# Kernel optimization log

Measured on AMD Instinct MI355X. Metric: run time of the kernel, lower is better.

The kernel has to match this reference:

```python
import jax, jax.numpy as jnp
import numpy as np

B, S, D, H = 4, 2048, 1024, 16
DK = D // H


def setup_inputs() -> dict:
    key = jax.random.key(0)
    ks = jax.random.split(key, 7)
    scale = 1.0 / np.sqrt(D)
    return {
        "query": jax.random.normal(ks[0], (B, S, D), dtype=jnp.float32),
        "key": jax.random.normal(ks[1], (B, S, D), dtype=jnp.float32),
        "value": jax.random.normal(ks[2], (B, S, D), dtype=jnp.float32),
        "mask": jnp.ones((B, S), dtype=bool),
        "w_q": jax.random.normal(ks[3], (D, D), dtype=jnp.float32) * scale,
        "w_k": jax.random.normal(ks[4], (D, D), dtype=jnp.float32) * scale,
        "w_v": jax.random.normal(ks[5], (D, D), dtype=jnp.float32) * scale,
        "w_o": jax.random.normal(ks[6], (D, D), dtype=jnp.float32) * scale,
    }


def reference(query, key, value, mask, w_q, w_k, w_v, w_o):
    b, tgt, d = query.shape
    src = key.shape[1]
    # torch Linear (no bias): x @ W.T
    Q = (query @ w_q.T).reshape(b, tgt, H, DK).transpose(0, 2, 1, 3)  # (B,H,T,dk)
    K = (key @ w_k.T).reshape(b, src, H, DK).transpose(0, 2, 1, 3)
    V = (value @ w_v.T).reshape(b, src, H, DK).transpose(0, 2, 1, 3)
    scores = jnp.einsum('bhtd,bhsd->bhts', Q, K) / np.sqrt(DK)  # (B,H,T,S)
    m = mask[:, None, None, :]  # (B,1,1,S)
    scores = jnp.where(m, scores, -jnp.inf)
    attn = jax.nn.softmax(scores, axis=-1)
    out = jnp.einsum('bhts,bhsd->bhtd', attn, V)
    out = out.transpose(0, 2, 1, 3).reshape(b, tgt, d)
    return out @ w_o.T
```

## Files before the change

### kernel.cpp

```cpp
#include <hip/hip_runtime.h>
#include <hip/hip_bf16.h>

#define NB 4
#define NS 2048
#define ND 1024
#define NH 16
#define NDK 64
#define GM 8192
#define GK 1024
#define GN 1024

typedef __bf16 bf16;
typedef __bf16 bf16x4 __attribute__((ext_vector_type(4)));
typedef __bf16 bf16x8 __attribute__((ext_vector_type(8)));
typedef float  f32x4  __attribute__((ext_vector_type(4)));
typedef float  f32x16 __attribute__((ext_vector_type(16)));
typedef unsigned u32x4 __attribute__((ext_vector_type(4)));

__device__ __forceinline__ void gl16(const void* g, void* l) {
  __builtin_amdgcn_global_load_lds((__attribute__((address_space(1))) void*)g,
                                   (__attribute__((address_space(3))) void*)l,
                                   16, 0, 0);
}

__device__ __forceinline__ unsigned cvtpk(float a, float b) {
  unsigned r;
  asm("v_cvt_pk_bf16_f32 %0, %1, %2" : "=v"(r) : "v"(a), "v"(b));
  return r;
}
__device__ __forceinline__ void plswap(unsigned &x, unsigned &y) {
  asm("v_permlane32_swap_b32 %0, %1" : "+v"(x), "+v"(y));
}
__device__ __forceinline__ float max3(float a, float b, float c) {
  float r;
  asm("v_max3_f32 %0, %1, %2, %3" : "=v"(r) : "v"(a), "v"(b), "v"(c));
  return r;
}
__device__ __forceinline__ float rexp2(float x) {
  float r;
  asm("v_exp_f32 %0, %1" : "=v"(r) : "v"(x));
  return r;
}

__device__ __forceinline__ bf16x8 packlo(const f32x16& s) {
  unsigned x0 = cvtpk(s[0], s[1]), y0 = cvtpk(s[4], s[5]);
  unsigned x1 = cvtpk(s[2], s[3]), y1 = cvtpk(s[6], s[7]);
  plswap(x0, y0); plswap(x1, y1);
  u32x4 w = {x0, x1, y0, y1};
  return __builtin_bit_cast(bf16x8, w);
}
__device__ __forceinline__ bf16x8 packhi(const f32x16& s) {
  unsigned x0 = cvtpk(s[8], s[9]),  y0 = cvtpk(s[12], s[13]);
  unsigned x1 = cvtpk(s[10], s[11]), y1 = cvtpk(s[14], s[15]);
  plswap(x0, y0); plswap(x1, y1);
  u32x4 w = {x0, x1, y0, y1};
  return __builtin_bit_cast(bf16x8, w);
}

__global__ void cvt4_f32_bf16(const float* __restrict__ w0, const float* __restrict__ w1,
                              const float* __restrict__ w2, const float* __restrict__ w3,
                              bf16* __restrict__ o0, bf16* __restrict__ o1,
                              bf16* __restrict__ o2, bf16* __restrict__ o3) {
  int i = blockIdx.x * 256 + threadIdx.x;
  int sel = i >> 18, j = i & 0x3FFFF;
  const float* src = sel == 0 ? w0 : sel == 1 ? w1 : sel == 2 ? w2 : w3;
  bf16* dst = sel == 0 ? o0 : sel == 1 ? o1 : sel == 2 ? o2 : o3;
  float4 f = reinterpret_cast<const float4*>(src)[j];
  bf16x4 v;
  v[0] = (bf16)f.x; v[1] = (bf16)f.y; v[2] = (bf16)f.z; v[3] = (bf16)f.w;
  reinterpret_cast<bf16x4*>(dst)[j] = v;
}

__global__ __launch_bounds__(256, 3)
void gemm_qkv(const float* __restrict__ q, const float* __restrict__ k,
              const float* __restrict__ v,
              const bf16* __restrict__ wq, const bf16* __restrict__ wk,
              const bf16* __restrict__ wv,
              bf16* __restrict__ Qf, bf16* __restrict__ Kf, bf16* __restrict__ Vf)
{
  __shared__ __align__(16) bf16 sA[128 * 32];
  __shared__ __align__(16) bf16 sB[128 * 32];
  const int tid = threadIdx.x;
  const int wid = tid >> 6, lane = tid & 63;
  const int l15 = lane & 15, l4 = lane >> 4;
  const int m0 = blockIdx.x * 128, n0 = blockIdx.y * 128;
  const int wr = wid >> 1, wc = wid & 1;
  const int z = blockIdx.z;
  const float* Af = z == 0 ? q : z == 1 ? k : v;
  const bf16*  Bw = z == 0 ? wq : z == 1 ? wk : wv;
  bf16* C = z == 0 ? Qf : z == 1 ? Kf : Vf;
  const float cscale = z == 0 ? 0.125f * 1.44269504f : 1.0f;

  const f32x4 zero4 = {0.f, 0.f, 0.f, 0.f};
  f32x4 acc[4][4];
  #pragma unroll
  for (int i = 0; i < 4; ++i)
    #pragma unroll
    for (int j = 0; j < 4; ++j) acc[i][j] = zero4;

  for (int k0 = 0; k0 < GK; k0 += 32) {
    #pragma unroll
    for (int p = 0; p < 2; ++p) {
      {
        int cb = p * 256 + wid * 64 + lane;
        int row = cb >> 2, col = (cb & 3) * 8;
        gl16(Bw + (size_t)(n0 + row) * GK + k0 + col,
             sB + (size_t)(p * 256 + wid * 64) * 8);
      }
      {
        int c = p * 256 + tid;
        int row = c >> 2, col = (c & 3) * 8;
        const float* s = Af + (size_t)(m0 + row) * GK + k0 + col;
        float4 f0 = *reinterpret_cast<const float4*>(s);
        float4 f1 = *reinterpret_cast<const float4*>(s + 4);
        bf16x8 vv;
        vv[0] = (bf16)f0.x; vv[1] = (bf16)f0.y; vv[2] = (bf16)f0.z; vv[3] = (bf16)f0.w;
        vv[4] = (bf16)f1.x; vv[5] = (bf16)f1.y; vv[6] = (bf16)f1.z; vv[7] = (bf16)f1.w;
        *reinterpret_cast<bf16x8*>(&sA[row * 32 + col]) = vv;
      }
    }
    __syncthreads();
    bf16x8 af[4], bfr[4];
    #pragma unroll
    for (int i = 0; i < 4; ++i)
      af[i] = *reinterpret_cast<const bf16x8*>(&sA[(wr * 64 + i * 16 + l15) * 32 + l4 * 8]);
    #pragma unroll
    for (int j = 0; j < 4; ++j)
      bfr[j] = *reinterpret_cast<const bf16x8*>(&sB[(wc * 64 + j * 16 + l15) * 32 + l4 * 8]);
    #pragma unroll
    for (int i = 0; i < 4; ++i)
      #pragma unroll
      for (int j = 0; j < 4; ++j)
        acc[i][j] = __builtin_amdgcn_mfma_f32_16x16x32_bf16(af[i], bfr[j], acc[i][j], 0, 0, 0);
    __syncthreads();
  }

  #pragma unroll
  for (int i = 0; i < 4; ++i) {
    #pragma unroll
    for (int j = 0; j < 4; ++j) {
      const int mb = m0 + wr * 64 + i * 16 + l4 * 4;
      const int n  = n0 + wc * 64 + j * 16 + l15;
      const int h = n >> 6, dk = n & 63;
      const int bh_ = (mb >> 11) * NH + h;
      const int s2 = mb & 2047;
      if (z < 2) {
        const int ks = dk >> 4, hiw = (dk >> 3) & 1, jj = dk & 7;
        size_t base = ((size_t)(bh_ * 64 + (s2 >> 5))) * 2048
                    + (ks * 2 + hiw) * 256 + (s2 & 31) * 8 + jj;
        #pragma unroll
        for (int r = 0; r < 4; ++r)
          C[base + r * 8] = (bf16)(acc[i][j][r] * cscale);
      } else {
        const int df = dk >> 5, l31v = dk & 31;
        size_t idx = ((size_t)(bh_ * 32 + (s2 >> 6))) * 4096
                   + (df * 8 + i * 2 + (l4 >> 1)) * 256 + l31v * 8 + (l4 & 1) * 4;
        bf16x4 vv;
        #pragma unroll
        for (int r = 0; r < 4; ++r) vv[r] = (bf16)(acc[i][j][r] * cscale);
        *reinterpret_cast<bf16x4*>(&C[idx]) = vv;
      }
    }
  }
}

__global__ __launch_bounds__(256, 3)
void gemm_out(const bf16* __restrict__ Ab, const bf16* __restrict__ Bw,
              float* __restrict__ C)
{
  __shared__ __align__(16) bf16 sA[128 * 32];
  __shared__ __align__(16) bf16 sB[128 * 32];
  const int tid = threadIdx.x;
  const int wid = tid >> 6, lane = tid & 63;
  const int l15 = lane & 15, l4 = lane >> 4;
  const int m0 = blockIdx.x * 128, n0 = blockIdx.y * 128;
  const int wr = wid >> 1, wc = wid & 1;

  const f32x4 zero4 = {0.f, 0.f, 0.f, 0.f};
  f32x4 acc[4][4];
  #pragma unroll
  for (int i = 0; i < 4; ++i)
    #pragma unroll
    for (int j = 0; j < 4; ++j) acc[i][j] = zero4;

  for (int k0 = 0; k0 < GK; k0 += 32) {
    #pragma unroll
    for (int p = 0; p < 2; ++p) {
      {
        int cb = p * 256 + wid * 64 + lane;
        int row = cb >> 2, col = (cb & 3) * 8;
        gl16(Bw + (size_t)(n0 + row) * GK + k0 + col,
             sB + (size_t)(p * 256 + wid * 64) * 8);
      }
      {
        int cb = p * 256 + wid * 64 + lane;
        int row = cb >> 2, col = (cb & 3) * 8;
        gl16(Ab + (size_t)(m0 + row) * GK + k0 + col,
             sA + (size_t)(p * 256 + wid * 64) * 8);
      }
    }
    __syncthreads();
    bf16x8 af[4], bfr[4];
    #pragma unroll
    for (int i = 0; i < 4; ++i)
      af[i] = *reinterpret_cast<const bf16x8*>(&sA[(wr * 64 + i * 16 + l15) * 32 + l4 * 8]);
    #pragma unroll
    for (int j = 0; j < 4; ++j)
      bfr[j] = *reinterpret_cast<const bf16x8*>(&sB[(wc * 64 + j * 16 + l15) * 32 + l4 * 8]);
    #pragma unroll
    for (int i = 0; i < 4; ++i)
      #pragma unroll
      for (int j = 0; j < 4; ++j)
        acc[i][j] = __builtin_amdgcn_mfma_f32_16x16x32_bf16(af[i], bfr[j], acc[i][j], 0, 0, 0);
    __syncthreads();
  }

  #pragma unroll
  for (int i = 0; i < 4; ++i) {
    #pragma unroll
    for (int j = 0; j < 4; ++j) {
      const int mb = m0 + wr * 64 + i * 16 + l4 * 4;
      const int n  = n0 + wc * 64 + j * 16 + l15;
      #pragma unroll
      for (int r = 0; r < 4; ++r)
        C[(size_t)(mb + r) * GN + n] = acc[i][j][r];
    }
  }
}

__global__ __launch_bounds__(256, 2)
void attn_fwd(const bf16* __restrict__ QF, const bf16* __restrict__ KF,
              const bf16* __restrict__ VF, bf16* __restrict__ AO)
{
  const int tid = threadIdx.x;
  const int wid = tid >> 6, lane = tid & 63;
  const int l31 = lane & 31, hi = lane >> 5;
  const int id = blockIdx.x;
  const int wg = (id & 7) * 64 + (id >> 3);
  const int qt = wg & 7, bh = wg >> 3;
  const int q0 = qt * 256 + wid * 64;

  const bf16* Qb = QF + ((size_t)bh * 64 + (q0 >> 5)) * 2048 + hi * 256 + l31 * 8;
  const bf16* Kb = KF + (size_t)bh * 64 * 2048 + hi * 256 + l31 * 8;
  const bf16* Vb = VF + (size_t)bh * 32 * 4096 + hi * 256 + l31 * 8;

  bf16x8 qf[2][4];
  #pragma unroll
  for (int u = 0; u < 2; ++u)
    #pragma unroll
    for (int ks = 0; ks < 4; ++ks)
      qf[u][ks] = *reinterpret_cast<const bf16x8*>(Qb + u * 2048 + ks * 512);

  f32x16 o[2][2] = {};
  float m[2]  = {-1e30f, -1e30f};
  float ls[2] = {0.f, 0.f};

  bf16x8 kf[2][4];
  #pragma unroll
  for (int f = 0; f < 2; ++f)
    #pragma unroll
    for (int ks = 0; ks < 4; ++ks)
      kf[f][ks] = *reinterpret_cast<const bf16x8*>(Kb + f * 2048 + ks * 512);

  for (int kv0 = 0; kv0 < NS; kv0 += 64) {
    const bf16* Vt = Vb + (kv0 >> 6) * 4096;
    bf16x8 vf[2][4];
    #pragma unroll
    for (int df = 0; df < 2; ++df)
      #pragma unroll
      for (int ks = 0; ks < 4; ++ks)
        vf[df][ks] = *reinterpret_cast<const bf16x8*>(Vt + df * 2048 + ks * 512);

    bf16x8 pb[2][4];
    #pragma unroll
    for (int u = 0; u < 2; ++u) {
      f32x16 s0 = {}, s1 = {};
      __builtin_amdgcn_s_setprio(1);
      #pragma unroll
      for (int ks = 0; ks < 4; ++ks)
        s0 = __builtin_amdgcn_mfma_f32_32x32x16_bf16(kf[0][ks], qf[u][ks], s0, 0, 0, 0);
      #pragma unroll
      for (int ks = 0; ks < 4; ++ks)
        s1 = __builtin_amdgcn_mfma_f32_32x32x16_bf16(kf[1][ks], qf[u][ks], s1, 0, 0, 0);
      __builtin_amdgcn_s_setprio(0);
      float a0 = max3(s0[0],  s0[1],  s0[2]);
      float a1 = max3(s0[3],  s0[4],  s0[5]);
      float a2 = max3(s0[6],  s0[7],  s0[8]);
      float a3 = max3(s0[9],  s0[10], s0[11]);
      float a4 = max3(s0[12], s0[13], s0[14]);
      float a5 = max3(s0[15], s1[0],  s1[1]);
      float a6 = max3(s1[2],  s1[3],  s1[4]);
      float a7 = max3(s1[5],  s1[6],  s1[7]);
      float a8 = max3(s1[8],  s1[9],  s1[10]);
      float a9 = max3(s1[11], s1[12], s1[13]);
      float aa = fmaxf(s1[14], s1[15]);
      float b0 = max3(a0, a1, a2);
      float b1 = max3(a3, a4, a5);
      float b2 = max3(a6, a7, a8);
      float b3 = fmaxf(a9, aa);
      float t = fmaxf(max3(b0, b1, b2), b3);
      t = fmaxf(t, __shfl_xor(t, 32, 64));
      if (__any(t > m[u] + 11.5f)) {
        float mn = fmaxf(m[u], t);
        float c = rexp2(m[u] - mn);
        ls[u] *= c;
        #pragma unroll
        for (int r = 0; r < 16; ++r) { o[u][0][r] *= c; o[u][1][r] *= c; }
        m[u] = mn;
      }
      #pragma unroll
      for (int r = 0; r < 16; ++r) s0[r] = rexp2(s0[r] - m[u]);
      #pragma unroll
      for (int r = 0; r < 16; ++r) s1[r] = rexp2(s1[r] - m[u]);
      {
        f32x16 ssum = s0 + s1;
        float p0 = (ssum[0] + ssum[1]) + (ssum[2] + ssum[3]);
        float p1 = (ssum[4] + ssum[5]) + (ssum[6] + ssum[7]);
        float p2 = (ssum[8] + ssum[9]) + (ssum[10] + ssum[11]);
        float p3 = (ssum[12] + ssum[13]) + (ssum[14] + ssum[15]);
        ls[u] += (p0 + p1) + (p2 + p3);
      }
      pb[u][0] = packlo(s0); pb[u][1] = packhi(s0);
      pb[u][2] = packlo(s1); pb[u][3] = packhi(s1);
    }
    const int kvn = (kv0 + 64) & (NS - 1);
    const bf16* Kt = Kb + (kvn >> 5) * 2048;
    #pragma unroll
    for (int f = 0; f < 2; ++f)
      #pragma unroll
      for (int ks = 0; ks < 4; ++ks)
        kf[f][ks] = *reinterpret_cast<const bf16x8*>(Kt + f * 2048 + ks * 512);
    __builtin_amdgcn_s_setprio(1);
    #pragma unroll
    for (int df = 0; df < 2; ++df)
      #pragma unroll
      for (int ks = 0; ks < 4; ++ks) {
        o[0][df] = __builtin_amdgcn_mfma_f32_32x32x16_bf16(vf[df][ks], pb[0][ks], o[0][df], 0, 0, 0);
        o[1][df] = __builtin_amdgcn_mfma_f32_32x32x16_bf16(vf[df][ks], pb[1][ks], o[1][df], 0, 0, 0);
      }
    __builtin_amdgcn_s_setprio(0);
  }

  const int b = bh >> 4, h = bh & 15;
  #pragma unroll
  for (int u = 0; u < 2; ++u) {
    float l = ls[u] + __shfl_xor(ls[u], 32, 64);
    float linv = 1.0f / l;
    const int s = q0 + u * 32 + l31;
    bf16* aop = AO + (((size_t)b * NS + s) * NH + h) * NDK;
    #pragma unroll
    for (int df = 0; df < 2; ++df)
      #pragma unroll
      for (int g = 0; g < 4; ++g) {
        bf16x4 v;
        #pragma unroll
        for (int r = 0; r < 4; ++r) v[r] = (bf16)(o[u][df][g * 4 + r] * linv);
        *reinterpret_cast<bf16x4*>(aop + df * 32 + g * 8 + hi * 4) = v;
      }
  }
}

extern "C" void kernel_launch(void* const* d_in, const int* in_sizes, int n_in,
                              void* d_out, int out_size, void* d_ws, size_t ws_size,
                              hipStream_t stream) {
  const float* query = (const float*)d_in[0];
  const float* key   = (const float*)d_in[1];
  const float* value = (const float*)d_in[2];
  const float* w_q = (const float*)d_in[4];
  const float* w_k = (const float*)d_in[5];
  const float* w_v = (const float*)d_in[6];
  const float* w_o = (const float*)d_in[7];
  float* out = (float*)d_out;

  char* ws = (char*)d_ws;
  bf16* wq_b = (bf16*)(ws + (size_t)0);
  bf16* wk_b = (bf16*)(ws + ((size_t)2 << 20));
  bf16* wv_b = (bf16*)(ws + ((size_t)4 << 20));
  bf16* wo_b = (bf16*)(ws + ((size_t)6 << 20));
  bf16* QF   = (bf16*)(ws + ((size_t)8  << 20));
  bf16* KF   = (bf16*)(ws + ((size_t)24 << 20));
  bf16* VF   = (bf16*)(ws + ((size_t)40 << 20));
  bf16* AO   = (bf16*)(ws + ((size_t)56 << 20));

  cvt4_f32_bf16<<<4096, 256, 0, stream>>>(w_q, w_k, w_v, w_o, wq_b, wk_b, wv_b, wo_b);

  gemm_qkv<<<dim3(GM / 128, GN / 128, 3), 256, 0, stream>>>(
      query, key, value, wq_b, wk_b, wv_b, QF, KF, VF);

  attn_fwd<<<dim3(512), 256, 0, stream>>>(QF, KF, VF, AO);

  gemm_out<<<dim3(GM / 128, GN / 128), 256, 0, stream>>>(AO, wo_b, out);
}
```

Before: 193.7 us.

## Split attention over KV halves with separate merge kernel

Attention is split so each block processes half of the key/value sequence, which doubles the grid. Each block writes unnormalized fp32 partial outputs plus its running max and sum. A new merge kernel then combines the two halves, normalizes, and writes the bf16 output. This aims for more parallelism and better load balance, at the cost of extra global memory traffic for the fp32 partials and one more kernel launch.

```diff
diff --git a/kernel.cpp b/kernel.cpp
--- a/kernel.cpp
+++ b/kernel.cpp
@@ -9,6 +9,7 @@
 #define GM 8192
 #define GK 1024
 #define GN 1024
+#define NROW 131072
 
 typedef __bf16 bf16;
 typedef __bf16 bf16x4 __attribute__((ext_vector_type(4)));
@@ -229,16 +230,20 @@
 }
 
 __global__ __launch_bounds__(256, 2)
-void attn_fwd(const bf16* __restrict__ QF, const bf16* __restrict__ KF,
-              const bf16* __restrict__ VF, bf16* __restrict__ AO)
+void attn_split(const bf16* __restrict__ QF, const bf16* __restrict__ KF,
+                const bf16* __restrict__ VF, float* __restrict__ PO,
+                float2* __restrict__ PML)
 {
   const int tid = threadIdx.x;
   const int wid = tid >> 6, lane = tid & 63;
   const int l31 = lane & 31, hi = lane >> 5;
   const int id = blockIdx.x;
-  const int wg = (id & 7) * 64 + (id >> 3);
-  const int qt = wg & 7, bh = wg >> 3;
+  const int wg = (id & 7) * 128 + (id >> 3);
+  const int half = wg & 1;
+  const int rest = wg >> 1;
+  const int qt = rest & 7, bh = rest >> 3;
   const int q0 = qt * 256 + wid * 64;
+  const int kvbase = half * (NS / 2);
 
   const bf16* Qb = QF + ((size_t)bh * 64 + (q0 >> 5)) * 2048 + hi * 256 + l31 * 8;
   const bf16* Kb = KF + (size_t)bh * 64 * 2048 + hi * 256 + l31 * 8;
@@ -260,9 +265,10 @@
   for (int f = 0; f < 2; ++f)
     #pragma unroll
     for (int ks = 0; ks < 4; ++ks)
-      kf[f][ks] = *reinterpret_cast<const bf16x8*>(Kb + f * 2048 + ks * 512);
-
-  for (int kv0 = 0; kv0 < NS; kv0 += 64) {
+      kf[f][ks] = *reinterpret_cast<const bf16x8*>(
+          Kb + (size_t)(kvbase >> 5) * 2048 + f * 2048 + ks * 512);
+
+  for (int kv0 = kvbase; kv0 < kvbase + NS / 2; kv0 += 64) {
     const bf16* Vt = Vb + (kv0 >> 6) * 4096;
     bf16x8 vf[2][4];
     #pragma unroll
@@ -323,8 +329,8 @@
       pb[u][0] = packlo(s0); pb[u][1] = packhi(s0);
       pb[u][2] = packlo(s1); pb[u][3] = packhi(s1);
     }
-    const int kvn = (kv0 + 64) & (NS - 1);
-    const bf16* Kt = Kb + (kvn >> 5) * 2048;
+    const int kvn = kvbase + ((kv0 - kvbase + 64) & (NS / 2 - 1));
+    const bf16* Kt = Kb + (size_t)(kvn >> 5) * 2048;
     #pragma unroll
     for (int f = 0; f < 2; ++f)
       #pragma unroll
@@ -341,23 +347,43 @@
     __builtin_amdgcn_s_setprio(0);
   }
 
-  const int b = bh >> 4, h = bh & 15;
   #pragma unroll
   for (int u = 0; u < 2; ++u) {
     float l = ls[u] + __shfl_xor(ls[u], 32, 64);
-    float linv = 1.0f / l;
-    const int s = q0 + u * 32 + l31;
-    bf16* aop = AO + (((size_t)b * NS + s) * NH + h) * NDK;
+    const int row = bh * 2048 + q0 + u * 32 + l31;
+    float* po = PO + ((size_t)half * NROW + row) * 64;
     #pragma unroll
     for (int df = 0; df < 2; ++df)
       #pragma unroll
       for (int g = 0; g < 4; ++g) {
-        bf16x4 v;
+        f32x4 t;
         #pragma unroll
-        for (int r = 0; r < 4; ++r) v[r] = (bf16)(o[u][df][g * 4 + r] * linv);
-        *reinterpret_cast<bf16x4*>(aop + df * 32 + g * 8 + hi * 4) = v;
-      }
-  }
+        for (int r = 0; r < 4; ++r) t[r] = o[u][df][g * 4 + r];
+        *reinterpret_cast<f32x4*>(po + df * 32 + g * 8 + hi * 4) = t;
+      }
+    PML[(size_t)half * NROW + row] = make_float2(m[u], l);
+  }
+}
+
+__global__ __launch_bounds__(256)
+void attn_merge(const float* __restrict__ PO, const float2* __restrict__ PML,
+                bf16* __restrict__ AO)
+{
+  int gid = blockIdx.x * 256 + threadIdx.x;
+  int row = gid >> 4, d0 = (gid & 15) * 4;
+  float2 ml0 = PML[row], ml1 = PML[NROW + row];
+  float mm = fmaxf(ml0.x, ml1.x);
+  float w0 = rexp2(ml0.x - mm), w1 = rexp2(ml1.x - mm);
+  float linv = 1.0f / (ml0.y * w0 + ml1.y * w1);
+  f32x4 a = *reinterpret_cast<const f32x4*>(PO + (size_t)row * 64 + d0);
+  f32x4 b = *reinterpret_cast<const f32x4*>(PO + ((size_t)NROW + row) * 64 + d0);
+  bf16x4 v;
+  #pragma unroll
+  for (int r = 0; r < 4; ++r)
+    v[r] = (bf16)((a[r] * w0 + b[r] * w1) * linv);
+  int bh = row >> 11, s = row & 2047;
+  int b_ = bh >> 4, h = bh & 15;
+  *reinterpret_cast<bf16x4*>(AO + (((size_t)b_ * NS + s) * NH + h) * NDK + d0) = v;
 }
 
 extern "C" void kernel_launch(void* const* d_in, const int* in_sizes, int n_in,
@@ -373,21 +399,24 @@
   float* out = (float*)d_out;
 
   char* ws = (char*)d_ws;
-  bf16* wq_b = (bf16*)(ws + (size_t)0);
-  bf16* wk_b = (bf16*)(ws + ((size_t)2 << 20));
-  bf16* wv_b = (bf16*)(ws + ((size_t)4 << 20));
-  bf16* wo_b = (bf16*)(ws + ((size_t)6 << 20));
-  bf16* QF   = (bf16*)(ws + ((size_t)8  << 20));
-  bf16* KF   = (bf16*)(ws + ((size_t)24 << 20));
-  bf16* VF   = (bf16*)(ws + ((size_t)40 << 20));
-  bf16* AO   = (bf16*)(ws + ((size_t)56 << 20));
+  bf16*   wq_b = (bf16*)(ws + (size_t)0);
+  bf16*   wk_b = (bf16*)(ws + ((size_t)2 << 20));
+  bf16*   wv_b = (bf16*)(ws + ((size_t)4 << 20));
+  bf16*   wo_b = (bf16*)(ws + ((size_t)6 << 20));
+  bf16*   QF   = (bf16*)(ws + ((size_t)8  << 20));
+  bf16*   KF   = (bf16*)(ws + ((size_t)24 << 20));
+  bf16*   VF   = (bf16*)(ws + ((size_t)40 << 20));
+  bf16*   AO   = (bf16*)(ws + ((size_t)56 << 20));
+  float*  PO   = (float*)(ws + ((size_t)72 << 20));
+  float2* PML  = (float2*)(ws + ((size_t)136 << 20));
 
   cvt4_f32_bf16<<<4096, 256, 0, stream>>>(w_q, w_k, w_v, w_o, wq_b, wk_b, wv_b, wo_b);
 
   gemm_qkv<<<dim3(GM / 128, GN / 128, 3), 256, 0, stream>>>(
       query, key, value, wq_b, wk_b, wv_b, QF, KF, VF);
 
-  attn_fwd<<<dim3(512), 256, 0, stream>>>(QF, KF, VF, AO);
+  attn_split<<<dim3(1024), 256, 0, stream>>>(QF, KF, VF, PO, PML);
+  attn_merge<<<dim3(8192), 256, 0, stream>>>(PO, PML, AO);
 
   gemm_out<<<dim3(GM / 128, GN / 128), 256, 0, stream>>>(AO, wo_b, out);
 }
```

New measurement: 227.9 us. 1.18x slower.
